# Kernel optimization log

Hardware: AMD Instinct MI355X
Metric: run time of the kernel (lower is better)

Reference implementation:

```python
import jax, jax.numpy as jnp
import numpy as np

B, S, D_IN, D_OUT = 4, 2048, 1024, 1024

def setup_inputs() -> dict:
    key = jax.random.key(0)
    k0, k1, k2, k3 = jax.random.split(key, 4)
    sc = 1.0 / np.sqrt(D_IN)
    return {
        "x": jax.random.normal(k0, (B, S, D_IN), dtype=jnp.float32),
        "wq": jax.random.normal(k1, (D_OUT, D_IN), dtype=jnp.float32) * sc,
        "wk": jax.random.normal(k2, (D_OUT, D_IN), dtype=jnp.float32) * sc,
        "wv": jax.random.normal(k3, (D_OUT, D_IN), dtype=jnp.float32) * sc,
    }

def reference(x, wq, wk, wv):
    # Linear (no bias): y = x @ W.T, W shaped [d_out, d_in]
    q = jnp.einsum("bsd,ed->bse", x, wq)
    k = jnp.einsum("bsd,ed->bse", x, wk)
    v = jnp.einsum("bsd,ed->bse", x, wv)
    scores = jnp.einsum("bqe,bke->bqk", q, k)  # [B,S,S]
    n = x.shape[1]
    causal = jnp.triu(jnp.ones((n, n), dtype=bool), k=1)  # True above diagonal -> masked
    scores = jnp.where(causal, -jnp.inf, scores)
    attn = jax.nn.softmax(scores / jnp.sqrt(jnp.asarray(k.shape[-1], scores.dtype)), axis=-1)
    # dropout p=0.0 -> identity
    return jnp.einsum("bqk,bke->bqe", attn, v)
```

## Files before the change

### kernel.cpp

```cpp
#include <hip/hip_runtime.h>

#define Bb 4
#define Ss 2048
#define Dd 1024

typedef unsigned short u16;
typedef __bf16 bf16x8 __attribute__((ext_vector_type(8)));
typedef float  f32x4  __attribute__((ext_vector_type(4)));

__device__ inline u16 f2bf(float f) {
  union { float f; unsigned u; } x; x.f = f;
  unsigned u = x.u;
  return (u16)((u + 0x7fffu + ((u >> 16) & 1u)) >> 16);
}
__device__ inline float bf2f(u16 h) {
  union { unsigned u; float f; } x; x.u = ((unsigned)h) << 16;
  return x.f;
}

__device__ static inline void gl_lds16(const u16* g, u16* l) {
  __builtin_amdgcn_global_load_lds((__attribute__((address_space(1))) const void*)g,
                                   (__attribute__((address_space(3))) void*)l,
                                   16, 0, 0);
}

__device__ static inline void qbar() {
  asm volatile("" ::: "memory");
  __builtin_amdgcn_s_barrier();
  asm volatile("" ::: "memory");
}

template <int GATEN>
__device__ __forceinline__ void qk_gate() {
  if constexpr (GATEN == 6) asm volatile("s_waitcnt vmcnt(6)" ::: "memory");
  else if constexpr (GATEN == 3) asm volatile("s_waitcnt vmcnt(3)" ::: "memory");
  else if constexpr (GATEN == 0) asm volatile("s_waitcnt vmcnt(0)" ::: "memory");
}

__global__ __launch_bounds__(256) void cast_all(const float* __restrict__ x,
                                                const float* __restrict__ wq,
                                                const float* __restrict__ wk,
                                                const float* __restrict__ wv,
                                                u16* __restrict__ xb,
                                                u16* __restrict__ wb,
                                                float* __restrict__ lsum) {
  int id = blockIdx.x;
  if (id < 8) {
    float4 z = {0.f, 0.f, 0.f, 0.f};
    ((float4*)lsum)[id * 256 + threadIdx.x] = z;
  }
  const float* src; u16* dst; int off;
  if (id < 2048) {
    src = x; dst = xb; off = id * 4096;
  } else {
    int wi = id - 2048;
    int w = wi >> 8;
    src = (w == 0) ? wq : (w == 1) ? wk : wv;
    dst = wb + (size_t)w * Dd * Dd;
    off = (wi & 255) * 4096;
  }
#pragma unroll
  for (int t = 0; t < 4; t++) {
    int i = off + t * 1024 + threadIdx.x * 4;
    float4 v = *(const float4*)(src + i);
    unsigned p0 = (unsigned)f2bf(v.x) | ((unsigned)f2bf(v.y) << 16);
    unsigned p1 = (unsigned)f2bf(v.z) | ((unsigned)f2bf(v.w) << 16);
    uint2 p; p.x = p0; p.y = p1;
    *(uint2*)(dst + i) = p;
  }
}

#define BM 128
#define BN 128

__device__ inline void gemm_tile(const u16* __restrict__ A, int lda,
                                 const u16* __restrict__ Bp, int ldb,
                                 int kBeg, int kEnd,
                                 u16* lds, f32x4 acc[4][4]) {
  u16* lA0 = lds;
  u16* lB0 = lds + 4096;
  u16* lA1 = lds + 8192;
  u16* lB1 = lds + 12288;
  const int tid  = threadIdx.x;
  const int lane = tid & 63, wave = tid >> 6;
  const int quad = lane >> 4, r16 = lane & 15;
  const int wm = (wave & 1) * 64, wn = (wave >> 1) * 64;
  const int r0 = tid >> 2, part = tid & 3;

  for (int k0 = kBeg; k0 < kEnd; k0 += 64) {
    __syncthreads();
#pragma unroll
    for (int q = 0; q < 2; q++) {
      int row = q * 64 + r0;
      int s8 = (q * 256 + tid) * 8;
      const u16* ga = A  + (size_t)row * lda + k0 + part * 8;
      const u16* gb = Bp + (size_t)row * ldb + k0 + part * 8;
      gl_lds16(ga,      lA0 + s8);
      gl_lds16(gb,      lB0 + s8);
      gl_lds16(ga + 32, lA1 + s8);
      gl_lds16(gb + 32, lB1 + s8);
    }
    __syncthreads();
#pragma unroll
    for (int h = 0; h < 2; h++) {
      const u16* la = h ? lA1 : lA0;
      const u16* lb = h ? lB1 : lB0;
      bf16x8 fa[4], fb[4];
#pragma unroll
      for (int t = 0; t < 4; t++)
        fa[t] = *(const bf16x8*)(la + (wm + t * 16 + r16) * 32 + quad * 8);
#pragma unroll
      for (int t = 0; t < 4; t++)
        fb[t] = *(const bf16x8*)(lb + (wn + t * 16 + r16) * 32 + quad * 8);
#pragma unroll
      for (int tm = 0; tm < 4; tm++)
#pragma unroll
        for (int tn = 0; tn < 4; tn++)
          acc[tm][tn] = __builtin_amdgcn_mfma_f32_16x16x32_bf16(fa[tm], fb[tn],
                                                                acc[tm][tn], 0, 0, 0);
    }
  }
}

#define QBK 32

__global__ __launch_bounds__(512, 1) void qkv_gemm3(const u16* __restrict__ xb,
                                                    const u16* __restrict__ wb,
                                                    u16* __restrict__ qkv) {
  __shared__ __align__(16) u16 sh[4 * 12288];

  const int id  = blockIdx.x;
  const int swz = (id & 7) * 96 + (id >> 3);
  const int zi  = swz >> 8;
  const int rem = swz & 255;
  const int mt  = rem >> 3, nt = rem & 7;
  const int row0 = mt * 256, col0 = nt * 128;
  const u16* A  = xb + (size_t)row0 * Dd;
  const u16* Bp = wb + (size_t)zi * Dd * Dd + (size_t)col0 * Dd;

  const int tid  = threadIdx.x;
  const int lane = tid & 63, wave = tid >> 6;
  const int wr = wave >> 1, wc = wave & 1;
  const int quad = lane >> 4, r16 = lane & 15;

  const int pA0 = tid, pA1 = tid + 512;
  const int r0a = pA0 >> 2, c0a = pA0 & 3;
  const int r1a = pA1 >> 2, c1a = pA1 & 3;
  const u16* aS0 = A  + (size_t)r0a * Dd + (size_t)((c0a ^ ((r0a >> 1) & 3)) * 8);
  const u16* aS1 = A  + (size_t)r1a * Dd + (size_t)((c1a ^ ((r1a >> 1) & 3)) * 8);
  const u16* bS0 = Bp + (size_t)r0a * Dd + (size_t)((c0a ^ ((r0a >> 1) & 3)) * 8);

  auto stg = [&](int S) {
    u16* d = sh + (S & 3) * 12288;
    gl_lds16(aS0 + (size_t)S * QBK, d + pA0 * 8);
    gl_lds16(aS1 + (size_t)S * QBK, d + pA1 * 8);
    gl_lds16(bS0 + (size_t)S * QBK, d + 8192 + pA0 * 8);
  };

  const int chq  = (quad ^ ((r16 >> 1) & 3)) * 8;
  const int idxA = (wr * 64 + r16) * 32 + chq;
  const int idxB = (wc * 64 + r16) * 32 + chq;

  f32x4 acc[4][4];
#pragma unroll
  for (int m = 0; m < 4; m++)
#pragma unroll
    for (int n = 0; n < 4; n++) acc[m][n] = (f32x4){0.f, 0.f, 0.f, 0.f};

#define QTILE(U, STG_S, GATEN)                                                 \
  {                                                                            \
    const u16* lA = sh + (U) * 12288;                                          \
    const u16* lB = lA + 8192;                                                 \
    bf16x8 fa[4], fb[4];                                                       \
    _Pragma("unroll") for (int m = 0; m < 4; m++)                              \
        fa[m] = *(const bf16x8*)(lA + idxA + m * 512);                         \
    _Pragma("unroll") for (int n = 0; n < 4; n++)                              \
        fb[n] = *(const bf16x8*)(lB + idxB + n * 512);                         \
    if ((STG_S) >= 0) stg(STG_S);                                              \
    qk_gate<GATEN>();                                                          \
    qbar();                                                                    \
    __builtin_amdgcn_s_setprio(1);                                             \
    _Pragma("unroll") for (int m = 0; m < 4; m++)                              \
      _Pragma("unroll") for (int n = 0; n < 4; n++)                            \
        acc[m][n] = __builtin_amdgcn_mfma_f32_16x16x32_bf16(fa[m], fb[n],      \
                                                            acc[m][n], 0, 0, 0); \
    __builtin_amdgcn_s_setprio(0);                                             \
    qbar();                                                                    \
  }

  stg(0); stg(1); stg(2);
  asm volatile("s_waitcnt vmcnt(6)" ::: "memory");
  qbar();

#pragma unroll 1
  for (int T = 0; T < 29; T++) QTILE(T & 3, T + 3, 6);
  QTILE(1, -1, 3);
  QTILE(2, -1, 0);
  QTILE(3, -1, -1);
#undef QTILE

  u16* out = qkv + (size_t)zi * ((size_t)Bb * Ss * Dd);
#pragma unroll
  for (int m = 0; m < 4; m++) {
    int rr = row0 + wr * 64 + m * 16 + quad * 4;
#pragma unroll
    for (int n = 0; n < 4; n++) {
      int cc = col0 + wc * 64 + n * 16 + r16;
#pragma unroll
      for (int r = 0; r < 4; r++)
        out[(size_t)(rr + r) * Dd + cc] = f2bf(acc[m][n][r]);
    }
  }
}

__global__ __launch_bounds__(256) void scores_fused(const u16* __restrict__ qb,
                                                    const u16* __restrict__ kb,
                                                    const u16* __restrict__ vb,
                                                    u16* __restrict__ sc,
                                                    u16* __restrict__ vt,
                                                    float* __restrict__ lsum) {
  __shared__ __align__(16) u16 shmem[16384];
  const int id = blockIdx.x;
  const int tid = threadIdx.x;

  if (id >= 544) {
    const int bid = id - 544;
    u16 (*t)[72] = (u16(*)[72])shmem;
    for (int u = bid; u < 2048; u += 480) {
      const int b = u >> 9, rem = u & 511;
      const int e0 = (rem >> 5) * 64, s0 = (rem & 31) * 64;
      const u16* src = vb + (size_t)b * Ss * Dd;
      u16* dst = vt + (size_t)b * Dd * Ss;
      if (u != bid) __syncthreads();
#pragma unroll
      for (int gg = tid; gg < 512; gg += 256) {
        int row = gg >> 3, prt = gg & 7;
        uint4 v = *(const uint4*)(src + (size_t)(s0 + row) * Dd + e0 + prt * 8);
        const u16* pv = (const u16*)&v;
#pragma unroll
        for (int jj = 0; jj < 8; jj++) t[prt * 8 + jj][row] = pv[jj];
      }
      __syncthreads();
#pragma unroll
      for (int gg = tid; gg < 512; gg += 256) {
        int ee = gg >> 3, prt = gg & 7;
        uint4 v = *(const uint4*)(&t[ee][prt * 8]);
        *(uint4*)(dst + (size_t)(e0 + ee) * Ss + s0 + prt * 8) = v;
      }
    }
    return;
  }

  const int xcd = id & 7, j = id >> 3;
  const int b = j / 17, tloc = j - b * 17;
  const int t = xcd * 17 + tloc;
  int it = (int)((sqrtf(8.f * (float)t + 1.f) - 1.f) * 0.5f);
  while ((it + 1) * (it + 2) / 2 <= t) it++;
  while (it * (it + 1) / 2 > t) it--;
  const int jt = t - it * (it + 1) / 2;

  const u16* A  = qb + (size_t)b * Ss * Dd + (size_t)it * BM * Dd;
  const u16* Bp = kb + (size_t)b * Ss * Dd + (size_t)jt * BN * Dd;
  f32x4 acc[4][4];
  const f32x4 zero = {0.f, 0.f, 0.f, 0.f};
#pragma unroll
  for (int tm = 0; tm < 4; tm++)
#pragma unroll
    for (int tn = 0; tn < 4; tn++) acc[tm][tn] = zero;

  gemm_tile(A, Dd, Bp, Dd, 0, Dd, shmem, acc);

  u16* out = sc + (size_t)b * Ss * Ss;
  float* lr = lsum + (size_t)b * Ss;
  const int lane = tid & 63, wave = tid >> 6;
  const int quad = lane >> 4, r16 = lane & 15;
  const int wm = (wave & 1) * 64, wn = (wave >> 1) * 64;
#pragma unroll
  for (int tm = 0; tm < 4; tm++) {
    float psum[4] = {0.f, 0.f, 0.f, 0.f};
#pragma unroll
    for (int tn = 0; tn < 4; tn++) {
      int rr = it * BM + wm + tm * 16 + quad * 4;
      int cc = jt * BN + wn + tn * 16 + r16;
#pragma unroll
      for (int r = 0; r < 4; r++) {
        float p = 0.f;
        u16 h = 0;
        if (cc <= rr + r) {
          h = f2bf(__expf(acc[tm][tn][r] * 0.03125f));
          p = bf2f(h);
        }
        out[(size_t)(rr + r) * Ss + cc] = h;
        psum[r] += p;
      }
    }
#pragma unroll
    for (int r = 0; r < 4; r++) {
      float s = psum[r];
      s += __shfl_xor(s, 1);
      s += __shfl_xor(s, 2);
      s += __shfl_xor(s, 4);
      s += __shfl_xor(s, 8);
      if (r16 == 0) {
        int row = it * BM + wm + tm * 16 + quad * 4 + r;
        atomicAdd(&lr[row], s);
      }
    }
  }
}

__global__ __launch_bounds__(256) void pv_gemm(const u16* __restrict__ sc,
                                               const u16* __restrict__ vt,
                                               const float* __restrict__ lsum,
                                               float* __restrict__ out) {
  __shared__ __align__(16) u16 shmem[16384];
  const int idx = blockIdx.x;
  const int xcd = idx & 7, slot = idx >> 3;
  const int qp = slot >> 3, col = slot & 7;
  const int b = qp & 3;
  const int it = (qp >> 2) ? (15 - xcd) : xcd;
  const int row0 = it * BM;
  const int col0 = col * BN;
  const u16* A  = sc + (size_t)b * Ss * Ss + (size_t)row0 * Ss;
  const u16* Bp = vt + (size_t)b * Dd * Ss + (size_t)col0 * Ss;
  f32x4 acc[4][4];
  const f32x4 zero = {0.f, 0.f, 0.f, 0.f};
#pragma unroll
  for (int tm = 0; tm < 4; tm++)
#pragma unroll
    for (int tn = 0; tn < 4; tn++) acc[tm][tn] = zero;

  gemm_tile(A, Ss, Bp, Ss, 0, row0 + BM, shmem, acc);

  float* o = out + (size_t)b * Ss * Dd;
  const float* lr = lsum + (size_t)b * Ss;
  const int lane = threadIdx.x & 63, wave = threadIdx.x >> 6;
  const int quad = lane >> 4, r16 = lane & 15;
  const int wm = (wave & 1) * 64, wn = (wave >> 1) * 64;
#pragma unroll
  for (int tm = 0; tm < 4; tm++) {
    int rbase = row0 + wm + tm * 16 + quad * 4;
    float s0 = 1.f / lr[rbase], s1 = 1.f / lr[rbase + 1];
    float s2 = 1.f / lr[rbase + 2], s3 = 1.f / lr[rbase + 3];
#pragma unroll
    for (int tn = 0; tn < 4; tn++) {
      int cc = col0 + wn + tn * 16 + r16;
      o[(size_t)(rbase + 0) * Dd + cc] = acc[tm][tn][0] * s0;
      o[(size_t)(rbase + 1) * Dd + cc] = acc[tm][tn][1] * s1;
      o[(size_t)(rbase + 2) * Dd + cc] = acc[tm][tn][2] * s2;
      o[(size_t)(rbase + 3) * Dd + cc] = acc[tm][tn][3] * s3;
    }
  }
}

extern "C" void kernel_launch(void* const* d_in, const int* in_sizes, int n_in,
                              void* d_out, int out_size, void* d_ws, size_t ws_size,
                              hipStream_t stream) {
  const float* x  = (const float*)d_in[0];
  const float* wq = (const float*)d_in[1];
  const float* wk = (const float*)d_in[2];
  const float* wv = (const float*)d_in[3];
  float* out = (float*)d_out;
  char* ws = (char*)d_ws;
  if (ws_size < 106987520u) return;

  u16* qkv  = (u16*)(ws);
  u16* sc   = (u16*)(ws + 50331648u);
  u16* xb   = (u16*)(ws + 83886080u);
  u16* vt   = xb;
  u16* wb   = (u16*)(ws + 100663296u);
  float* lsum = (float*)(ws + 106954752u);

  const size_t nQ = (size_t)Bb * Ss * Dd;

  cast_all<<<2816, 256, 0, stream>>>(x, wq, wk, wv, xb, wb, lsum);
  qkv_gemm3<<<768, 512, 0, stream>>>(xb, wb, qkv);
  scores_fused<<<1024, 256, 0, stream>>>(qkv, qkv + nQ, qkv + 2 * nQ, sc, vt, lsum);
  pv_gemm<<<512, 256, 0, stream>>>(sc, vt, lsum, out);
}
```

Before: 238.7 us.

## Fuse QKV projection into one wide-tile GEMM over concatenated weights

```diff
diff --git a/kernel.cpp b/kernel.cpp
--- a/kernel.cpp
+++ b/kernel.cpp
@@ -32,8 +32,7 @@
 
 template <int GATEN>
 __device__ __forceinline__ void qk_gate() {
-  if constexpr (GATEN == 6) asm volatile("s_waitcnt vmcnt(6)" ::: "memory");
-  else if constexpr (GATEN == 3) asm volatile("s_waitcnt vmcnt(3)" ::: "memory");
+  if constexpr (GATEN == 5) asm volatile("s_waitcnt vmcnt(5)" ::: "memory");
   else if constexpr (GATEN == 0) asm volatile("s_waitcnt vmcnt(0)" ::: "memory");
 }
 
@@ -123,92 +122,100 @@
 }
 
 #define QBK 32
-
-__global__ __launch_bounds__(512, 1) void qkv_gemm3(const u16* __restrict__ xb,
+#define FBUF 20480
+
+__global__ __launch_bounds__(512, 2) void qkv_fused(const u16* __restrict__ xb,
                                                     const u16* __restrict__ wb,
                                                     u16* __restrict__ qkv) {
-  __shared__ __align__(16) u16 sh[4 * 12288];
+  __shared__ __align__(16) u16 sh[3 * FBUF];
 
   const int id  = blockIdx.x;
-  const int swz = (id & 7) * 96 + (id >> 3);
-  const int zi  = swz >> 8;
-  const int rem = swz & 255;
-  const int mt  = rem >> 3, nt = rem & 7;
-  const int row0 = mt * 256, col0 = nt * 128;
+  const int nt  = id & 7, mt = id >> 3;
+  const int row0 = mt * 256, col0 = nt * 384;
   const u16* A  = xb + (size_t)row0 * Dd;
-  const u16* Bp = wb + (size_t)zi * Dd * Dd + (size_t)col0 * Dd;
+  const u16* Bp = wb + (size_t)col0 * Dd;
 
   const int tid  = threadIdx.x;
   const int lane = tid & 63, wave = tid >> 6;
-  const int wr = wave >> 1, wc = wave & 1;
+  const int wr = wave >> 2, wc = wave & 3;
   const int quad = lane >> 4, r16 = lane & 15;
 
-  const int pA0 = tid, pA1 = tid + 512;
-  const int r0a = pA0 >> 2, c0a = pA0 & 3;
-  const int r1a = pA1 >> 2, c1a = pA1 & 3;
-  const u16* aS0 = A  + (size_t)r0a * Dd + (size_t)((c0a ^ ((r0a >> 1) & 3)) * 8);
-  const u16* aS1 = A  + (size_t)r1a * Dd + (size_t)((c1a ^ ((r1a >> 1) & 3)) * 8);
-  const u16* bS0 = Bp + (size_t)r0a * Dd + (size_t)((c0a ^ ((r0a >> 1) & 3)) * 8);
+  const int rA0 = tid >> 2,          cA0 = tid & 3;
+  const int rA1 = (tid + 512) >> 2,  cA1 = tid & 3;
+  const int rB2 = (tid + 1024) >> 2;
+  const u16* aS0 = A  + (size_t)rA0 * Dd + (size_t)((cA0 ^ ((rA0 >> 1) & 3)) * 8);
+  const u16* aS1 = A  + (size_t)rA1 * Dd + (size_t)((cA1 ^ ((rA1 >> 1) & 3)) * 8);
+  const u16* bS0 = Bp + (size_t)rA0 * Dd + (size_t)((cA0 ^ ((rA0 >> 1) & 3)) * 8);
+  const u16* bS1 = Bp + (size_t)rA1 * Dd + (size_t)((cA1 ^ ((rA1 >> 1) & 3)) * 8);
+  const u16* bS2 = Bp + (size_t)rB2 * Dd + (size_t)((cA0 ^ ((rB2 >> 1) & 3)) * 8);
 
   auto stg = [&](int S) {
-    u16* d = sh + (S & 3) * 12288;
-    gl_lds16(aS0 + (size_t)S * QBK, d + pA0 * 8);
-    gl_lds16(aS1 + (size_t)S * QBK, d + pA1 * 8);
-    gl_lds16(bS0 + (size_t)S * QBK, d + 8192 + pA0 * 8);
+    u16* d = sh + (S % 3) * FBUF;
+    const size_t ko = (size_t)S * QBK;
+    gl_lds16(aS0 + ko, d + tid * 8);
+    gl_lds16(aS1 + ko, d + (tid + 512) * 8);
+    u16* db = d + 8192;
+    gl_lds16(bS0 + ko, db + tid * 8);
+    gl_lds16(bS1 + ko, db + (tid + 512) * 8);
+    gl_lds16(bS2 + ko, db + (tid + 1024) * 8);
   };
 
   const int chq  = (quad ^ ((r16 >> 1) & 3)) * 8;
-  const int idxA = (wr * 64 + r16) * 32 + chq;
-  const int idxB = (wc * 64 + r16) * 32 + chq;
-
-  f32x4 acc[4][4];
-#pragma unroll
-  for (int m = 0; m < 4; m++)
-#pragma unroll
-    for (int n = 0; n < 4; n++) acc[m][n] = (f32x4){0.f, 0.f, 0.f, 0.f};
-
-#define QTILE(U, STG_S, GATEN)                                                 \
+  const int idxA = (wr * 128 + r16) * 32 + chq;
+  const int idxB = 8192 + (wc * 96 + r16) * 32 + chq;
+
+  f32x4 acc[8][6];
+#pragma unroll
+  for (int m = 0; m < 8; m++)
+#pragma unroll
+    for (int n = 0; n < 6; n++) acc[m][n] = (f32x4){0.f, 0.f, 0.f, 0.f};
+
+#define FPH(T_, DOSTG, GATEN)                                                  \
   {                                                                            \
-    const u16* lA = sh + (U) * 12288;                                          \
-    const u16* lB = lA + 8192;                                                 \
-    bf16x8 fa[4], fb[4];                                                       \
+    const u16* bf = sh + ((T_) % 3) * FBUF;                                    \
+    bf16x8 fb[6], fa[4];                                                       \
+    _Pragma("unroll") for (int n = 0; n < 6; n++)                              \
+        fb[n] = *(const bf16x8*)(bf + idxB + n * 512);                         \
     _Pragma("unroll") for (int m = 0; m < 4; m++)                              \
-        fa[m] = *(const bf16x8*)(lA + idxA + m * 512);                         \
-    _Pragma("unroll") for (int n = 0; n < 4; n++)                              \
-        fb[n] = *(const bf16x8*)(lB + idxB + n * 512);                         \
-    if ((STG_S) >= 0) stg(STG_S);                                              \
+        fa[m] = *(const bf16x8*)(bf + idxA + m * 512);                         \
+    if (DOSTG) stg((T_) + 2);                                                  \
     qk_gate<GATEN>();                                                          \
     qbar();                                                                    \
     __builtin_amdgcn_s_setprio(1);                                             \
     _Pragma("unroll") for (int m = 0; m < 4; m++)                              \
-      _Pragma("unroll") for (int n = 0; n < 4; n++)                            \
+      _Pragma("unroll") for (int n = 0; n < 6; n++)                            \
         acc[m][n] = __builtin_amdgcn_mfma_f32_16x16x32_bf16(fa[m], fb[n],      \
                                                             acc[m][n], 0, 0, 0); \
+    _Pragma("unroll") for (int m = 0; m < 4; m++)                              \
+        fa[m] = *(const bf16x8*)(bf + idxA + (m + 4) * 512);                   \
+    _Pragma("unroll") for (int m = 0; m < 4; m++)                              \
+      _Pragma("unroll") for (int n = 0; n < 6; n++)                            \
+        acc[m + 4][n] = __builtin_amdgcn_mfma_f32_16x16x32_bf16(fa[m], fb[n],  \
+                                                                acc[m + 4][n], 0, 0, 0); \
     __builtin_amdgcn_s_setprio(0);                                             \
     qbar();                                                                    \
   }
 
-  stg(0); stg(1); stg(2);
-  asm volatile("s_waitcnt vmcnt(6)" ::: "memory");
+  stg(0); stg(1);
+  qk_gate<5>();
   qbar();
 
 #pragma unroll 1
-  for (int T = 0; T < 29; T++) QTILE(T & 3, T + 3, 6);
-  QTILE(1, -1, 3);
-  QTILE(2, -1, 0);
-  QTILE(3, -1, -1);
-#undef QTILE
-
-  u16* out = qkv + (size_t)zi * ((size_t)Bb * Ss * Dd);
-#pragma unroll
-  for (int m = 0; m < 4; m++) {
-    int rr = row0 + wr * 64 + m * 16 + quad * 4;
-#pragma unroll
-    for (int n = 0; n < 4; n++) {
-      int cc = col0 + wc * 64 + n * 16 + r16;
+  for (int T = 0; T < 30; T++) FPH(T, true, 5);
+  FPH(30, false, 0);
+  FPH(31, false, -1);
+#undef FPH
+
+#pragma unroll
+  for (int m = 0; m < 8; m++) {
+    int rr = row0 + wr * 128 + m * 16 + quad * 4;
+#pragma unroll
+    for (int n = 0; n < 6; n++) {
+      int cc = col0 + wc * 96 + n * 16 + r16;
+      u16* o = qkv + (size_t)(cc >> 10) * ((size_t)Bb * Ss * Dd) + (cc & 1023);
 #pragma unroll
       for (int r = 0; r < 4; r++)
-        out[(size_t)(rr + r) * Dd + cc] = f2bf(acc[m][n][r]);
+        o[(size_t)(rr + r) * Dd] = f2bf(acc[m][n][r]);
     }
   }
 }
@@ -374,7 +381,7 @@
   const size_t nQ = (size_t)Bb * Ss * Dd;
 
   cast_all<<<2816, 256, 0, stream>>>(x, wq, wk, wv, xb, wb, lsum);
-  qkv_gemm3<<<768, 512, 0, stream>>>(xb, wb, qkv);
+  qkv_fused<<<256, 512, 0, stream>>>(xb, wb, qkv);
   scores_fused<<<1024, 256, 0, stream>>>(qkv, qkv + nQ, qkv + 2 * nQ, sc, vt, lsum);
   pv_gemm<<<512, 256, 0, stream>>>(sc, vt, lsum, out);
 }
```

Result: no change. 242.8 us (+1.7%).
